# Optimization experiments

Measured on AMD Instinct MI355X. Metric: run time of the kernel, lower is better.

The kernel has to match this reference:

```python
import jax, jax.numpy as jnp
import numpy as np

EMBED_DIM = 128
B, SQ, SKV = 16, 2048, 2048


def setup_inputs() -> dict:
    key = jax.random.key(0)
    ks = jax.random.split(key, 8)
    d = EMBED_DIM
    scale = 1.0 / np.sqrt(d)
    return {
        "x": jax.random.normal(ks[0], (B, SQ, d), dtype=jnp.float32),
        "y": jax.random.normal(ks[1], (B, SKV, d), dtype=jnp.float32),
        "Wq": jax.random.normal(ks[2], (d, d), dtype=jnp.float32) * scale,
        "bq": jax.random.normal(ks[3], (d,), dtype=jnp.float32) * 0.02,
        "Wk": jax.random.normal(ks[4], (d, d), dtype=jnp.float32) * scale,
        "bk": jax.random.normal(ks[5], (d,), dtype=jnp.float32) * 0.02,
        "Wv": jax.random.normal(ks[6], (d, d), dtype=jnp.float32) * scale,
        "bv": jax.random.normal(ks[7], (d,), dtype=jnp.float32) * 0.02,
    }


def reference(x, y, Wq, bq, Wk, bk, Wv, bv):
    # Linear projections (torch Linear: x @ W.T + b; here W stored as [in,out])
    q = x @ Wq + bq            # [B, SQ, d]
    k = y @ Wk + bk            # [B, SKV, d]
    v = y @ Wv + bv            # [B, SKV, d]
    # Source scales by q.size(-1)**0.5 = sqrt(embed_dim)
    inv_scale = 1.0 / jnp.sqrt(jnp.asarray(q.shape[-1], q.dtype))
    scores = jnp.einsum("bqd,bkd->bqk", q, k) * inv_scale  # [B, SQ, SKV]
    attn = jax.nn.softmax(scores, axis=-1)
    return jnp.einsum("bqk,bkd->bqd", attn, v)
```

## Files before the change

### kernel.cpp

```cpp
#include <hip/hip_runtime.h>
#include <hip/hip_bf16.h>

typedef unsigned short ushort_t;
typedef __attribute__((ext_vector_type(8))) short short8;
typedef __attribute__((ext_vector_type(4))) float f32x4;
typedef __attribute__((ext_vector_type(16))) float f32x16;

#define MFMA16(a, b, c) __builtin_amdgcn_mfma_f32_16x16x32_bf16((a), (b), (c), 0, 0, 0)
#define MFMA32(a, b, c) __builtin_amdgcn_mfma_f32_32x32x16_bf16((a), (b), (c), 0, 0, 0)

__device__ __forceinline__ ushort_t f2bf(float f) {
    return __builtin_bit_cast(ushort_t, __float2bfloat16(f));
}

#define CVTPK(lo, hi) ({ unsigned int r_; \
    asm("v_cvt_pk_bf16_f32 %0, %1, %2" : "=v"(r_) : "v"(lo), "v"(hi)); r_; })

__device__ __forceinline__ void gl_lds16(const void* g, void* l) {
    __builtin_amdgcn_global_load_lds((const __attribute__((address_space(1))) void*)g,
                                     (__attribute__((address_space(3))) void*)l, 16, 0, 0);
}

__global__ __launch_bounds__(256) void wt_kernel(
    const float* __restrict__ Wq, const float* __restrict__ Wk, const float* __restrict__ Wv,
    ushort_t* __restrict__ WTq, ushort_t* __restrict__ WTk, ushort_t* __restrict__ WTv)
{
    __shared__ __align__(16) ushort_t wt2[128 * 24];

    const int mat  = blockIdx.x >> 3;
    const int slab = blockIdx.x & 7;
    const float* W = (mat == 0) ? Wq : (mat == 1) ? Wk : Wv;
    ushort_t*   WT = (mat == 0) ? WTq : (mat == 1) ? WTk : WTv;

    const int t = threadIdx.x;
    #pragma unroll
    for (int i = 0; i < 2; ++i) {
        int idx = t + i * 256;
        int kloc = idx >> 5;
        int c0   = (idx & 31) * 4;
        f32x4 v = ((const f32x4*)(W + (size_t)(slab * 16) * 128))[idx];
        #pragma unroll
        for (int j = 0; j < 4; ++j)
            wt2[(c0 + j) * 24 + kloc] = f2bf(v[j]);
    }
    __syncthreads();
    const int r    = t >> 1;
    const int half = t & 1;
    short8 v8 = *(const short8*)&wt2[r * 24 + half * 8];
    *(short8*)(WT + r * 128 + slab * 16 + half * 8) = v8;
}

__global__ __launch_bounds__(256) void proj3(
    const float* __restrict__ x, const float* __restrict__ y,
    const ushort_t* __restrict__ WTq, const float* __restrict__ bq,
    const ushort_t* __restrict__ WTk, const float* __restrict__ bk,
    const ushort_t* __restrict__ WTv, const float* __restrict__ bv,
    ushort_t* __restrict__ Qd, ushort_t* __restrict__ Kd, ushort_t* __restrict__ VTd,
    float qscale)
{
    __shared__ __align__(16) char smem[34816];

    const int t = threadIdx.x;
    const int mat = blockIdx.x >> 9;
    const int pb  = blockIdx.x & 511;
    const float* src = (mat == 0) ? x : y;

    const int w  = t >> 6;
    const int l  = t & 63;
    const int lg = l >> 4;
    const int ln = l & 15;
    const int acol = lg * 8;

    {
        const char* srcb = (const char*)(src + (size_t)(pb * 64) * 128);
        #pragma unroll
        for (int i = 0; i < 8; ++i) {
            int off = i * 4096 + w * 1024 + l * 16;
            int soff = off ^ (((off >> 9) & 7) << 4);
            gl_lds16(srcb + soff, smem + i * 4096 + w * 1024);
        }
    }
    __syncthreads();

    short8 afrag[4];
    {
        const int row = w * 16 + ln;
        const int sw = (row & 7) << 4;
        #pragma unroll
        for (int kc = 0; kc < 4; ++kc) {
            int off0 = row * 512 + lg * 32 + kc * 128;
            f32x4 a0 = *(const f32x4*)(smem + (off0 ^ sw));
            f32x4 a1 = *(const f32x4*)(smem + ((off0 + 16) ^ sw));
            short8 a;
            #pragma unroll
            for (int j = 0; j < 4; ++j) { a[j] = (short)f2bf(a0[j]); a[4 + j] = (short)f2bf(a1[j]); }
            afrag[kc] = a;
        }
    }
    __syncthreads();

    const ushort_t* WT = (mat == 0) ? WTq : (mat == 1) ? WTk : WTv;
    const float*    bb = (mat == 0) ? bq  : (mat == 1) ? bk  : bv;
    const float     sc = (mat == 0) ? qscale : 1.0f;

    if (mat < 2) {
        ushort_t* tile = (ushort_t*)smem;
        #pragma unroll
        for (int ct = 0; ct < 8; ++ct) {
            f32x4 acc = {0.f, 0.f, 0.f, 0.f};
            const int c = ct * 16 + ln;
            #pragma unroll
            for (int kc = 0; kc < 4; ++kc) {
                short8 bfr = *(const short8*)(WT + c * 128 + kc * 32 + acol);
                acc = MFMA16(afrag[kc], bfr, acc);
            }
            float bvv = bb[c];
            #pragma unroll
            for (int reg = 0; reg < 4; ++reg)
                tile[(w * 16 + lg * 4 + reg) * 144 + c] = f2bf((acc[reg] + bvv) * sc);
        }
        __syncthreads();
        const int row = t >> 2, ch = t & 3;
        ushort_t* dst1 = (mat == 0 ? Qd : Kd) + (size_t)(pb * 64 + row) * 128 + ch * 32;
        #pragma unroll
        for (int j = 0; j < 4; ++j)
            *(short8*)(dst1 + j * 8) = *(const short8*)&tile[row * 144 + ch * 32 + j * 8];
    } else {
        ushort_t* vt = (ushort_t*)smem;
        #pragma unroll
        for (int ct = 0; ct < 8; ++ct) {
            f32x4 acc = {0.f, 0.f, 0.f, 0.f};
            const int c = ct * 16 + ln;
            #pragma unroll
            for (int kc = 0; kc < 4; ++kc) {
                short8 bfr = *(const short8*)(WT + c * 128 + kc * 32 + acol);
                acc = MFMA16(afrag[kc], bfr, acc);
            }
            float bvv = bb[c];
            #pragma unroll
            for (int reg = 0; reg < 4; ++reg) {
                int rloc = w * 16 + lg * 4 + reg;
                int byte = (c * 128 + rloc * 2) ^ ((c & 7) << 4);
                *(ushort_t*)((char*)vt + byte) = f2bf(acc[reg] + bvv);
            }
        }
        __syncthreads();
        const int r0b = pb * 64;
        const int b   = r0b >> 11;
        const int kv0 = r0b & 2047;
        const int c    = t >> 1;
        const int half = t & 1;
        ushort_t* dst = VTd + (size_t)b * 128 * 2048 + (size_t)c * 2048 + kv0 + half * 32;
        #pragma unroll
        for (int j = 0; j < 4; ++j) {
            int byte = (c * 128 + (half * 32 + j * 8) * 2) ^ ((c & 7) << 4);
            *(short8*)(dst + j * 8) = *(const short8*)((const char*)vt + byte);
        }
    }
}

#define KVBLK 64
#define NT (2048 / KVBLK)
__global__ __launch_bounds__(256) void attn_kernel(
    const ushort_t* __restrict__ Q, const ushort_t* __restrict__ K,
    const ushort_t* __restrict__ VT, float* __restrict__ out)
{
    __shared__ __align__(16) char smem_[49152];

    const int t = threadIdx.x;
    const int bid = (int)blockIdx.x;
    const int wg = (bid & 7) * 64 + (bid >> 3);
    const int b  = wg >> 5;
    const int q0blk = (wg & 31) * 64;

    const char* Kb  = (const char*)(K  + (size_t)b * 2048 * 128);
    const char* VTb = (const char*)(VT + (size_t)b * 128 * 2048);
    const ushort_t* Qb = Q + (size_t)b * 2048 * 128;

    const int w   = t >> 6;
    const int qg  = w >> 1;
    const int kvh = w & 1;
    const int l  = t & 63;
    const int lq = l & 31;
    const int h  = l >> 5;
    const int q0 = q0blk + qg * 32;

    short8 qfrag[8];
    {
        const ushort_t* qp = Qb + (size_t)(q0 + lq) * 128 + h * 8;
        #pragma unroll
        for (int kc = 0; kc < 8; ++kc)
            qfrag[kc] = *(const short8*)(qp + kc * 16);
    }

    f32x16 o[4];
    #pragma unroll
    for (int db = 0; db < 4; ++db)
        #pragma unroll
        for (int i = 0; i < 16; ++i) o[db][i] = 0.f;
    f32x16 ls;
    #pragma unroll
    for (int i = 0; i < 16; ++i) ls[i] = 0.f;

    auto stageK = [&](char* kd, int kt) {
        const char* kb = Kb + (size_t)kt * KVBLK * 256;
        #pragma unroll
        for (int i = 0; i < 4; ++i) {
            int base = w * 4096 + i * 1024;
            int p = base + l * 16;
            int pl = p ^ (((p >> 8) & 15) << 4);
            gl_lds16(kb + pl, kd + base);
        }
    };
    auto stageV = [&](char* vd, int kt) {
        const int kv2 = kt * KVBLK * 2;
        #pragma unroll
        for (int i = 0; i < 4; ++i) {
            int base = w * 4096 + i * 1024;
            int p = base + l * 16;
            int pl = p ^ (((p >> 8) & 15) << 4);
            int dv = ((pl >> 8) << 1) | ((pl >> 7) & 1);
            gl_lds16(VTb + (size_t)dv * 4096 + kv2 + (pl & 127), vd + base);
        }
    };

    char* bK = smem_;
    char* bV = smem_ + 16384;
    char* bN = smem_ + 32768;

    stageK(bK, 0);
    stageV(bV, 0);

    for (int kt = 0; kt < NT; ++kt) {
        const int ktn = (kt + 1 < NT) ? kt + 1 : 0;

        asm volatile("s_waitcnt vmcnt(4)" ::: "memory");
        __builtin_amdgcn_s_barrier();
        stageK(bN, ktn);

        f32x16 s;
        #pragma unroll
        for (int i = 0; i < 16; ++i) s[i] = 0.f;
        const int krow = kvh * 32 + lq;
        const int ksw = (krow & 15) << 4;
        __builtin_amdgcn_s_setprio(1);
        #pragma unroll
        for (int kc = 0; kc < 8; ++kc) {
            int col = (h * 16 + kc * 32) ^ ksw;
            short8 kf = *(const short8*)(bK + krow * 256 + col);
            s = MFMA32(kf, qfrag[kc], s);
        }
        __builtin_amdgcn_s_setprio(0);

        #pragma unroll
        for (int i = 0; i < 16; ++i) s[i] = __builtin_exp2f(s[i]);
        #pragma unroll
        for (int i = 0; i < 16; ++i) ls[i] += s[i];

        short8 pf[2];
        {
            auto pack2 = [&](int a, short8& outf) {
                unsigned u0 = CVTPK(s[a * 8 + 0], s[a * 8 + 1]);
                unsigned u1 = CVTPK(s[a * 8 + 2], s[a * 8 + 3]);
                unsigned u2 = CVTPK(s[a * 8 + 4], s[a * 8 + 5]);
                unsigned u3 = CVTPK(s[a * 8 + 6], s[a * 8 + 7]);
                asm("v_permlane32_swap_b32 %0, %1" : "+v"(u0), "+v"(u2));
                asm("v_permlane32_swap_b32 %0, %1" : "+v"(u1), "+v"(u3));
                union { unsigned wds[4]; short8 s8; } f;
                f.wds[0] = u0; f.wds[1] = u1; f.wds[2] = u2; f.wds[3] = u3;
                outf = f.s8;
            };
            pack2(0, pf[0]);
            pack2(1, pf[1]);
        }

        asm volatile("s_waitcnt vmcnt(4)" ::: "memory");
        __builtin_amdgcn_s_barrier();
        stageV(bK, ktn);

        __builtin_amdgcn_s_setprio(1);
        #pragma unroll
        for (int db = 0; db < 4; ++db) {
            int d = db * 32 + lq;
            int vrow = d >> 1;
            int vsw = (vrow & 15) << 4;
            #pragma unroll
            for (int ks = 0; ks < 2; ++ks) {
                int colb = ((d & 1) << 7) | (kvh * 64 + ks * 32 + h * 16);
                short8 vf = *(const short8*)(bV + vrow * 256 + (colb ^ vsw));
                o[db] = MFMA32(vf, pf[ks], o[db]);
            }
        }
        __builtin_amdgcn_s_setprio(0);

        char* tmp = bK; bK = bN; bN = bV; bV = tmp;
    }

    asm volatile("s_waitcnt vmcnt(0)" ::: "memory");

    float lsum;
    {
        float a8[8];
        #pragma unroll
        for (int i = 0; i < 8; ++i) a8[i] = ls[i] + ls[i + 8];
        #pragma unroll
        for (int i = 0; i < 4; ++i) a8[i] += a8[i + 4];
        lsum = (a8[0] + a8[1]) + (a8[2] + a8[3]);
    }
    lsum += __shfl_xor(lsum, 32);

    __syncthreads();
    float* mrg = (float*)smem_;
    const int mo = qg * 4224 + lq * 132;
    const int mlb = 8448;

    if (kvh == 1) {
        #pragma unroll
        for (int db = 0; db < 4; ++db) {
            #pragma unroll
            for (int rq = 0; rq < 4; ++rq) {
                f32x4 v4;
                #pragma unroll
                for (int j = 0; j < 4; ++j) v4[j] = o[db][rq * 4 + j];
                *(f32x4*)&mrg[mo + db * 32 + rq * 8 + 4 * h] = v4;
            }
        }
        if (h == 0) mrg[mlb + qg * 64 + lq] = lsum;
    }
    __syncthreads();
    if (kvh == 0) {
        float inv = 1.0f / (lsum + mrg[mlb + qg * 64 + lq]);
        float* ob = out + (size_t)b * 2048 * 128 + (size_t)(q0 + lq) * 128;
        #pragma unroll
        for (int db = 0; db < 4; ++db) {
            #pragma unroll
            for (int rq = 0; rq < 4; ++rq) {
                f32x4 p4 = *(const f32x4*)&mrg[mo + db * 32 + rq * 8 + 4 * h];
                f32x4 st;
                #pragma unroll
                for (int j = 0; j < 4; ++j)
                    st[j] = (o[db][rq * 4 + j] + p4[j]) * inv;
                *(f32x4*)(ob + db * 32 + rq * 8 + 4 * h) = st;
            }
        }
    }
}

extern "C" void kernel_launch(void* const* d_in, const int* in_sizes, int n_in,
                              void* d_out, int out_size, void* d_ws, size_t ws_size,
                              hipStream_t stream) {
    (void)in_sizes; (void)n_in; (void)out_size; (void)ws_size;
    const float* x  = (const float*)d_in[0];
    const float* y  = (const float*)d_in[1];
    const float* Wq = (const float*)d_in[2];
    const float* bq = (const float*)d_in[3];
    const float* Wk = (const float*)d_in[4];
    const float* bk = (const float*)d_in[5];
    const float* Wv = (const float*)d_in[6];
    const float* bv = (const float*)d_in[7];
    float* out = (float*)d_out;

    ushort_t* wtq = (ushort_t*)d_out;
    ushort_t* wtk = wtq + 16384;
    ushort_t* wtv = wtk + 16384;

    ushort_t* qws  = (ushort_t*)d_ws;
    ushort_t* kws  = qws + (size_t)32768 * 128;
    ushort_t* vtws = kws + (size_t)32768 * 128;

    const float qscale = (float)(1.4426950408889634 / 11.313708498984761);

    wt_kernel<<<24, 256, 0, stream>>>(Wq, Wk, Wv, wtq, wtk, wtv);
    proj3<<<1536, 256, 0, stream>>>(x, y, wtq, bq, wtk, bk, wtv, bv, qws, kws, vtws, qscale);
    attn_kernel<<<512, 256, 0, stream>>>(qws, kws, vtws, out);
}
```

Baseline: 95.49 us.

## Fuse weight transpose, projections and attention into one persistent kernel

Merges the three launches (weight transpose, QKV projection, attention) into a single 512-block kernel separated by software grid barriers built on atomic counters, with each block handling three projection jobs in a loop. The goal is to remove launch overhead and the idle gaps between dependent kernels. In exchange it adds a memset launch for the counters and two global barriers that spin with sleeps. It also depends on all 512 blocks being co-resident, which is not guaranteed and could deadlock or time out otherwise. Projection work now runs at 512-block parallelism instead of 1536, and the fallback counter location sits inside the output buffer.

```diff
diff --git a/kernel.cpp b/kernel.cpp
--- a/kernel.cpp
+++ b/kernel.cpp
@@ -21,161 +21,177 @@
                                      (__attribute__((address_space(3))) void*)l, 16, 0, 0);
 }
 
-__global__ __launch_bounds__(256) void wt_kernel(
-    const float* __restrict__ Wq, const float* __restrict__ Wk, const float* __restrict__ Wv,
-    ushort_t* __restrict__ WTq, ushort_t* __restrict__ WTk, ushort_t* __restrict__ WTv)
-{
-    __shared__ __align__(16) ushort_t wt2[128 * 24];
-
-    const int mat  = blockIdx.x >> 3;
-    const int slab = blockIdx.x & 7;
-    const float* W = (mat == 0) ? Wq : (mat == 1) ? Wk : Wv;
-    ushort_t*   WT = (mat == 0) ? WTq : (mat == 1) ? WTk : WTv;
-
-    const int t = threadIdx.x;
-    #pragma unroll
-    for (int i = 0; i < 2; ++i) {
-        int idx = t + i * 256;
-        int kloc = idx >> 5;
-        int c0   = (idx & 31) * 4;
-        f32x4 v = ((const f32x4*)(W + (size_t)(slab * 16) * 128))[idx];
-        #pragma unroll
-        for (int j = 0; j < 4; ++j)
-            wt2[(c0 + j) * 24 + kloc] = f2bf(v[j]);
-    }
+__device__ __forceinline__ void grid_barrier(unsigned* cnt, unsigned target) {
+    __threadfence();
     __syncthreads();
-    const int r    = t >> 1;
-    const int half = t & 1;
-    short8 v8 = *(const short8*)&wt2[r * 24 + half * 8];
-    *(short8*)(WT + r * 128 + slab * 16 + half * 8) = v8;
-}
-
-__global__ __launch_bounds__(256) void proj3(
-    const float* __restrict__ x, const float* __restrict__ y,
-    const ushort_t* __restrict__ WTq, const float* __restrict__ bq,
-    const ushort_t* __restrict__ WTk, const float* __restrict__ bk,
-    const ushort_t* __restrict__ WTv, const float* __restrict__ bv,
-    ushort_t* __restrict__ Qd, ushort_t* __restrict__ Kd, ushort_t* __restrict__ VTd,
-    float qscale)
-{
-    __shared__ __align__(16) char smem[34816];
-
-    const int t = threadIdx.x;
-    const int mat = blockIdx.x >> 9;
-    const int pb  = blockIdx.x & 511;
-    const float* src = (mat == 0) ? x : y;
-
-    const int w  = t >> 6;
-    const int l  = t & 63;
-    const int lg = l >> 4;
-    const int ln = l & 15;
-    const int acol = lg * 8;
-
-    {
-        const char* srcb = (const char*)(src + (size_t)(pb * 64) * 128);
-        #pragma unroll
-        for (int i = 0; i < 8; ++i) {
-            int off = i * 4096 + w * 1024 + l * 16;
-            int soff = off ^ (((off >> 9) & 7) << 4);
-            gl_lds16(srcb + soff, smem + i * 4096 + w * 1024);
+    if (threadIdx.x == 0) {
+        __hip_atomic_fetch_add(cnt, 1u, __ATOMIC_ACQ_REL, __HIP_MEMORY_SCOPE_AGENT);
+        long spins = 0;
+        while (__hip_atomic_load(cnt, __ATOMIC_ACQUIRE, __HIP_MEMORY_SCOPE_AGENT) < target
+               && ++spins < (1L << 28)) {
+            __builtin_amdgcn_s_sleep(8);
         }
     }
     __syncthreads();
-
-    short8 afrag[4];
-    {
-        const int row = w * 16 + ln;
-        const int sw = (row & 7) << 4;
-        #pragma unroll
-        for (int kc = 0; kc < 4; ++kc) {
-            int off0 = row * 512 + lg * 32 + kc * 128;
-            f32x4 a0 = *(const f32x4*)(smem + (off0 ^ sw));
-            f32x4 a1 = *(const f32x4*)(smem + ((off0 + 16) ^ sw));
-            short8 a;
-            #pragma unroll
-            for (int j = 0; j < 4; ++j) { a[j] = (short)f2bf(a0[j]); a[4 + j] = (short)f2bf(a1[j]); }
-            afrag[kc] = a;
-        }
-    }
-    __syncthreads();
-
-    const ushort_t* WT = (mat == 0) ? WTq : (mat == 1) ? WTk : WTv;
-    const float*    bb = (mat == 0) ? bq  : (mat == 1) ? bk  : bv;
-    const float     sc = (mat == 0) ? qscale : 1.0f;
-
-    if (mat < 2) {
-        ushort_t* tile = (ushort_t*)smem;
-        #pragma unroll
-        for (int ct = 0; ct < 8; ++ct) {
-            f32x4 acc = {0.f, 0.f, 0.f, 0.f};
-            const int c = ct * 16 + ln;
-            #pragma unroll
-            for (int kc = 0; kc < 4; ++kc) {
-                short8 bfr = *(const short8*)(WT + c * 128 + kc * 32 + acol);
-                acc = MFMA16(afrag[kc], bfr, acc);
-            }
-            float bvv = bb[c];
-            #pragma unroll
-            for (int reg = 0; reg < 4; ++reg)
-                tile[(w * 16 + lg * 4 + reg) * 144 + c] = f2bf((acc[reg] + bvv) * sc);
-        }
-        __syncthreads();
-        const int row = t >> 2, ch = t & 3;
-        ushort_t* dst1 = (mat == 0 ? Qd : Kd) + (size_t)(pb * 64 + row) * 128 + ch * 32;
-        #pragma unroll
-        for (int j = 0; j < 4; ++j)
-            *(short8*)(dst1 + j * 8) = *(const short8*)&tile[row * 144 + ch * 32 + j * 8];
-    } else {
-        ushort_t* vt = (ushort_t*)smem;
-        #pragma unroll
-        for (int ct = 0; ct < 8; ++ct) {
-            f32x4 acc = {0.f, 0.f, 0.f, 0.f};
-            const int c = ct * 16 + ln;
-            #pragma unroll
-            for (int kc = 0; kc < 4; ++kc) {
-                short8 bfr = *(const short8*)(WT + c * 128 + kc * 32 + acol);
-                acc = MFMA16(afrag[kc], bfr, acc);
-            }
-            float bvv = bb[c];
-            #pragma unroll
-            for (int reg = 0; reg < 4; ++reg) {
-                int rloc = w * 16 + lg * 4 + reg;
-                int byte = (c * 128 + rloc * 2) ^ ((c & 7) << 4);
-                *(ushort_t*)((char*)vt + byte) = f2bf(acc[reg] + bvv);
-            }
-        }
-        __syncthreads();
-        const int r0b = pb * 64;
-        const int b   = r0b >> 11;
-        const int kv0 = r0b & 2047;
-        const int c    = t >> 1;
-        const int half = t & 1;
-        ushort_t* dst = VTd + (size_t)b * 128 * 2048 + (size_t)c * 2048 + kv0 + half * 32;
-        #pragma unroll
-        for (int j = 0; j < 4; ++j) {
-            int byte = (c * 128 + (half * 32 + j * 8) * 2) ^ ((c & 7) << 4);
-            *(short8*)(dst + j * 8) = *(const short8*)((const char*)vt + byte);
-        }
-    }
+    __threadfence();
 }
 
 #define KVBLK 64
 #define NT (2048 / KVBLK)
-__global__ __launch_bounds__(256) void attn_kernel(
-    const ushort_t* __restrict__ Q, const ushort_t* __restrict__ K,
-    const ushort_t* __restrict__ VT, float* __restrict__ out)
+
+__global__ __launch_bounds__(256) void fused_kernel(
+    const float* __restrict__ x, const float* __restrict__ y,
+    const float* __restrict__ Wq, const float* __restrict__ bq,
+    const float* __restrict__ Wk, const float* __restrict__ bk,
+    const float* __restrict__ Wv, const float* __restrict__ bv,
+    ushort_t* __restrict__ WT,
+    ushort_t* __restrict__ Qd, ushort_t* __restrict__ Kd, ushort_t* __restrict__ VTd,
+    float* __restrict__ out, unsigned* __restrict__ cnt, float qscale)
 {
     __shared__ __align__(16) char smem_[49152];
 
     const int t = threadIdx.x;
     const int bid = (int)blockIdx.x;
+
+    if (bid < 24) {
+        ushort_t* wt2 = (ushort_t*)smem_;
+        const int mat  = bid >> 3;
+        const int slab = bid & 7;
+        const float* W = (mat == 0) ? Wq : (mat == 1) ? Wk : Wv;
+        ushort_t*   WTm = WT + mat * 16384;
+
+        #pragma unroll
+        for (int i = 0; i < 2; ++i) {
+            int idx = t + i * 256;
+            int kloc = idx >> 5;
+            int c0   = (idx & 31) * 4;
+            f32x4 v = ((const f32x4*)(W + (size_t)(slab * 16) * 128))[idx];
+            #pragma unroll
+            for (int j = 0; j < 4; ++j)
+                wt2[(c0 + j) * 24 + kloc] = f2bf(v[j]);
+        }
+        __syncthreads();
+        const int r    = t >> 1;
+        const int half = t & 1;
+        short8 v8 = *(const short8*)&wt2[r * 24 + half * 8];
+        *(short8*)(WTm + r * 128 + slab * 16 + half * 8) = v8;
+    }
+
+    grid_barrier(&cnt[0], 512);
+
+    {
+        const int w  = t >> 6;
+        const int l  = t & 63;
+        const int lg = l >> 4;
+        const int ln = l & 15;
+        const int acol = lg * 8;
+
+        for (int j = 0; j < 3; ++j) {
+            const int job = bid + j * 512;
+            const int mat = job >> 9;
+            const int pb  = job & 511;
+            const float* src = (mat == 0) ? x : y;
+
+            __syncthreads();
+
+            {
+                const char* srcb = (const char*)(src + (size_t)(pb * 64) * 128);
+                #pragma unroll
+                for (int i = 0; i < 8; ++i) {
+                    int off = i * 4096 + w * 1024 + l * 16;
+                    int soff = off ^ (((off >> 9) & 7) << 4);
+                    gl_lds16(srcb + soff, smem_ + i * 4096 + w * 1024);
+                }
+            }
+            __syncthreads();
+
+            short8 afrag[4];
+            {
+                const int row = w * 16 + ln;
+                const int sw = (row & 7) << 4;
+                #pragma unroll
+                for (int kc = 0; kc < 4; ++kc) {
+                    int off0 = row * 512 + lg * 32 + kc * 128;
+                    f32x4 a0 = *(const f32x4*)(smem_ + (off0 ^ sw));
+                    f32x4 a1 = *(const f32x4*)(smem_ + ((off0 + 16) ^ sw));
+                    short8 a;
+                    #pragma unroll
+                    for (int jj = 0; jj < 4; ++jj) { a[jj] = (short)f2bf(a0[jj]); a[4 + jj] = (short)f2bf(a1[jj]); }
+                    afrag[kc] = a;
+                }
+            }
+            __syncthreads();
+
+            const ushort_t* WTm = WT + mat * 16384;
+            const float*    bb = (mat == 0) ? bq : (mat == 1) ? bk : bv;
+            const float     sc = (mat == 0) ? qscale : 1.0f;
+
+            if (mat < 2) {
+                ushort_t* tile = (ushort_t*)smem_;
+                #pragma unroll
+                for (int ct = 0; ct < 8; ++ct) {
+                    f32x4 acc = {0.f, 0.f, 0.f, 0.f};
+                    const int c = ct * 16 + ln;
+                    #pragma unroll
+                    for (int kc = 0; kc < 4; ++kc) {
+                        short8 bfr = *(const short8*)(WTm + c * 128 + kc * 32 + acol);
+                        acc = MFMA16(afrag[kc], bfr, acc);
+                    }
+                    float bvv = bb[c];
+                    #pragma unroll
+                    for (int reg = 0; reg < 4; ++reg)
+                        tile[(w * 16 + lg * 4 + reg) * 144 + c] = f2bf((acc[reg] + bvv) * sc);
+                }
+                __syncthreads();
+                const int row = t >> 2, ch = t & 3;
+                ushort_t* dst1 = (mat == 0 ? Qd : Kd) + (size_t)(pb * 64 + row) * 128 + ch * 32;
+                #pragma unroll
+                for (int jj = 0; jj < 4; ++jj)
+                    *(short8*)(dst1 + jj * 8) = *(const short8*)&tile[row * 144 + ch * 32 + jj * 8];
+            } else {
+                ushort_t* vt = (ushort_t*)smem_;
+                #pragma unroll
+                for (int ct = 0; ct < 8; ++ct) {
+                    f32x4 acc = {0.f, 0.f, 0.f, 0.f};
+                    const int c = ct * 16 + ln;
+                    #pragma unroll
+                    for (int kc = 0; kc < 4; ++kc) {
+                        short8 bfr = *(const short8*)(WTm + c * 128 + kc * 32 + acol);
+                        acc = MFMA16(afrag[kc], bfr, acc);
+                    }
+                    float bvv = bb[c];
+                    #pragma unroll
+                    for (int reg = 0; reg < 4; ++reg) {
+                        int rloc = w * 16 + lg * 4 + reg;
+                        int byte = (c * 128 + rloc * 2) ^ ((c & 7) << 4);
+                        *(ushort_t*)((char*)vt + byte) = f2bf(acc[reg] + bvv);
+                    }
+                }
+                __syncthreads();
+                const int r0b = pb * 64;
+                const int b   = r0b >> 11;
+                const int kv0 = r0b & 2047;
+                const int c    = t >> 1;
+                const int half = t & 1;
+                ushort_t* dst = VTd + (size_t)b * 128 * 2048 + (size_t)c * 2048 + kv0 + half * 32;
+                #pragma unroll
+                for (int jj = 0; jj < 4; ++jj) {
+                    int byte = (c * 128 + (half * 32 + jj * 8) * 2) ^ ((c & 7) << 4);
+                    *(short8*)(dst + jj * 8) = *(const short8*)((const char*)vt + byte);
+                }
+            }
+        }
+    }
+
+    grid_barrier(&cnt[1], 512);
+
     const int wg = (bid & 7) * 64 + (bid >> 3);
     const int b  = wg >> 5;
     const int q0blk = (wg & 31) * 64;
 
-    const char* Kb  = (const char*)(K  + (size_t)b * 2048 * 128);
-    const char* VTb = (const char*)(VT + (size_t)b * 128 * 2048);
-    const ushort_t* Qb = Q + (size_t)b * 2048 * 128;
+    const char* Kb  = (const char*)(Kd  + (size_t)b * 2048 * 128);
+    const char* VTb = (const char*)(VTd + (size_t)b * 128 * 2048);
+    const ushort_t* Qb = Qd + (size_t)b * 2048 * 128;
 
     const int w   = t >> 6;
     const int qg  = w >> 1;
@@ -349,7 +365,7 @@
 extern "C" void kernel_launch(void* const* d_in, const int* in_sizes, int n_in,
                               void* d_out, int out_size, void* d_ws, size_t ws_size,
                               hipStream_t stream) {
-    (void)in_sizes; (void)n_in; (void)out_size; (void)ws_size;
+    (void)in_sizes; (void)n_in; (void)out_size;
     const float* x  = (const float*)d_in[0];
     const float* y  = (const float*)d_in[1];
     const float* Wq = (const float*)d_in[2];
@@ -360,17 +376,22 @@
     const float* bv = (const float*)d_in[7];
     float* out = (float*)d_out;
 
-    ushort_t* wtq = (ushort_t*)d_out;
-    ushort_t* wtk = wtq + 16384;
-    ushort_t* wtv = wtk + 16384;
-
     ushort_t* qws  = (ushort_t*)d_ws;
     ushort_t* kws  = qws + (size_t)32768 * 128;
     ushort_t* vtws = kws + (size_t)32768 * 128;
+    const size_t used = (size_t)3 * 32768 * 128 * sizeof(ushort_t);
+    unsigned* cnt;
+    if (ws_size >= used + 256) {
+        cnt = (unsigned*)((char*)d_ws + used);
+    } else {
+        cnt = (unsigned*)((char*)d_out + 196608);
+    }
+
+    ushort_t* wt = (ushort_t*)d_out;
 
     const float qscale = (float)(1.4426950408889634 / 11.313708498984761);
 
-    wt_kernel<<<24, 256, 0, stream>>>(Wq, Wk, Wv, wtq, wtk, wtv);
-    proj3<<<1536, 256, 0, stream>>>(x, y, wtq, bq, wtk, bk, wtv, bv, qws, kws, vtws, qscale);
-    attn_kernel<<<512, 256, 0, stream>>>(qws, kws, vtws, out);
-}
+    hipMemsetAsync(cnt, 0, 8, stream);
+    fused_kernel<<<512, 256, 0, stream>>>(x, y, Wq, bq, Wk, bk, Wv, bv,
+                                          wt, qws, kws, vtws, out, cnt, qscale);
+}
```

Measured after the change: 321.3 us. +236.5%, slower.

## Fuse weight transpose into projection and deepen attention K/V prefetch pipeline

Applied to the files above, without the earlier changes.

Removes the separate weight-transpose kernel. Each projection block now converts and transposes the full fp32 weight matrix into swizzled bf16 LDS itself, which saves one launch but repeats that work in all 1536 blocks and raises LDS to 64KB. The attention kernel goes from a 3-buffer to a 5-buffer rotation, prefetching K/V two tiles ahead with a looser vmcnt wait to hide global-load latency. This raises attention LDS to 80KB, which may cut the number of blocks resident per CU.

```diff
diff --git a/kernel.cpp b/kernel.cpp
--- a/kernel.cpp
+++ b/kernel.cpp
@@ -21,49 +21,23 @@
                                      (__attribute__((address_space(3))) void*)l, 16, 0, 0);
 }
 
-__global__ __launch_bounds__(256) void wt_kernel(
-    const float* __restrict__ Wq, const float* __restrict__ Wk, const float* __restrict__ Wv,
-    ushort_t* __restrict__ WTq, ushort_t* __restrict__ WTk, ushort_t* __restrict__ WTv)
-{
-    __shared__ __align__(16) ushort_t wt2[128 * 24];
-
-    const int mat  = blockIdx.x >> 3;
-    const int slab = blockIdx.x & 7;
-    const float* W = (mat == 0) ? Wq : (mat == 1) ? Wk : Wv;
-    ushort_t*   WT = (mat == 0) ? WTq : (mat == 1) ? WTk : WTv;
-
-    const int t = threadIdx.x;
-    #pragma unroll
-    for (int i = 0; i < 2; ++i) {
-        int idx = t + i * 256;
-        int kloc = idx >> 5;
-        int c0   = (idx & 31) * 4;
-        f32x4 v = ((const f32x4*)(W + (size_t)(slab * 16) * 128))[idx];
-        #pragma unroll
-        for (int j = 0; j < 4; ++j)
-            wt2[(c0 + j) * 24 + kloc] = f2bf(v[j]);
-    }
-    __syncthreads();
-    const int r    = t >> 1;
-    const int half = t & 1;
-    short8 v8 = *(const short8*)&wt2[r * 24 + half * 8];
-    *(short8*)(WT + r * 128 + slab * 16 + half * 8) = v8;
-}
-
 __global__ __launch_bounds__(256) void proj3(
     const float* __restrict__ x, const float* __restrict__ y,
-    const ushort_t* __restrict__ WTq, const float* __restrict__ bq,
-    const ushort_t* __restrict__ WTk, const float* __restrict__ bk,
-    const ushort_t* __restrict__ WTv, const float* __restrict__ bv,
+    const float* __restrict__ Wq, const float* __restrict__ bq,
+    const float* __restrict__ Wk, const float* __restrict__ bk,
+    const float* __restrict__ Wv, const float* __restrict__ bv,
     ushort_t* __restrict__ Qd, ushort_t* __restrict__ Kd, ushort_t* __restrict__ VTd,
     float qscale)
 {
-    __shared__ __align__(16) char smem[34816];
+    __shared__ __align__(16) char smem[65536];
 
     const int t = threadIdx.x;
     const int mat = blockIdx.x >> 9;
     const int pb  = blockIdx.x & 511;
     const float* src = (mat == 0) ? x : y;
+    const float* W   = (mat == 0) ? Wq : (mat == 1) ? Wk : Wv;
+    const float* bb  = (mat == 0) ? bq : (mat == 1) ? bk : bv;
+    const float  sc  = (mat == 0) ? qscale : 1.0f;
 
     const int w  = t >> 6;
     const int l  = t & 63;
@@ -80,6 +54,21 @@
             gl_lds16(srcb + soff, smem + i * 4096 + w * 1024);
         }
     }
+
+    char* wt = smem + 32768;
+    #pragma unroll
+    for (int i = 0; i < 16; ++i) {
+        int idx = t + i * 256;
+        int k  = idx >> 5;
+        int c0 = (idx & 31) * 4;
+        f32x4 v = ((const f32x4*)W)[idx];
+        #pragma unroll
+        for (int j = 0; j < 4; ++j) {
+            int c = c0 + j;
+            int byte = (c * 256 + k * 2) ^ ((c & 7) << 4);
+            *(ushort_t*)(wt + byte) = f2bf(v[j]);
+        }
+    }
     __syncthreads();
 
     short8 afrag[4];
@@ -99,10 +88,6 @@
     }
     __syncthreads();
 
-    const ushort_t* WT = (mat == 0) ? WTq : (mat == 1) ? WTk : WTv;
-    const float*    bb = (mat == 0) ? bq  : (mat == 1) ? bk  : bv;
-    const float     sc = (mat == 0) ? qscale : 1.0f;
-
     if (mat < 2) {
         ushort_t* tile = (ushort_t*)smem;
         #pragma unroll
@@ -111,7 +96,8 @@
             const int c = ct * 16 + ln;
             #pragma unroll
             for (int kc = 0; kc < 4; ++kc) {
-                short8 bfr = *(const short8*)(WT + c * 128 + kc * 32 + acol);
+                int byte = (c * 256 + (kc * 32 + acol) * 2) ^ ((c & 7) << 4);
+                short8 bfr = *(const short8*)(wt + byte);
                 acc = MFMA16(afrag[kc], bfr, acc);
             }
             float bvv = bb[c];
@@ -133,7 +119,8 @@
             const int c = ct * 16 + ln;
             #pragma unroll
             for (int kc = 0; kc < 4; ++kc) {
-                short8 bfr = *(const short8*)(WT + c * 128 + kc * 32 + acol);
+                int byte = (c * 256 + (kc * 32 + acol) * 2) ^ ((c & 7) << 4);
+                short8 bfr = *(const short8*)(wt + byte);
                 acc = MFMA16(afrag[kc], bfr, acc);
             }
             float bvv = bb[c];
@@ -165,7 +152,7 @@
     const ushort_t* __restrict__ Q, const ushort_t* __restrict__ K,
     const ushort_t* __restrict__ VT, float* __restrict__ out)
 {
-    __shared__ __align__(16) char smem_[49152];
+    __shared__ __align__(16) char smem_[81920];
 
     const int t = threadIdx.x;
     const int bid = (int)blockIdx.x;
@@ -224,19 +211,23 @@
         }
     };
 
-    char* bK = smem_;
-    char* bV = smem_ + 16384;
-    char* bN = smem_ + 32768;
-
-    stageK(bK, 0);
-    stageV(bV, 0);
+    char* p0 = smem_;
+    char* p1 = smem_ + 16384;
+    char* p2 = smem_ + 32768;
+    char* p3 = smem_ + 49152;
+    char* p4 = smem_ + 65536;
+
+    stageK(p0, 0);
+    stageV(p1, 0);
+    stageK(p2, 1);
+    stageV(p3, 1);
 
     for (int kt = 0; kt < NT; ++kt) {
-        const int ktn = (kt + 1 < NT) ? kt + 1 : 0;
-
-        asm volatile("s_waitcnt vmcnt(4)" ::: "memory");
+        const int kt2 = (kt + 2 < NT) ? kt + 2 : 0;
+
+        asm volatile("s_waitcnt vmcnt(12)" ::: "memory");
         __builtin_amdgcn_s_barrier();
-        stageK(bN, ktn);
+        stageK(p4, kt2);
 
         f32x16 s;
         #pragma unroll
@@ -247,7 +238,7 @@
         #pragma unroll
         for (int kc = 0; kc < 8; ++kc) {
             int col = (h * 16 + kc * 32) ^ ksw;
-            short8 kf = *(const short8*)(bK + krow * 256 + col);
+            short8 kf = *(const short8*)(p0 + krow * 256 + col);
             s = MFMA32(kf, qfrag[kc], s);
         }
         __builtin_amdgcn_s_setprio(0);
@@ -274,9 +265,9 @@
             pack2(1, pf[1]);
         }
 
-        asm volatile("s_waitcnt vmcnt(4)" ::: "memory");
+        asm volatile("s_waitcnt vmcnt(12)" ::: "memory");
         __builtin_amdgcn_s_barrier();
-        stageV(bK, ktn);
+        stageV(p0, kt2);
 
         __builtin_amdgcn_s_setprio(1);
         #pragma unroll
@@ -287,13 +278,14 @@
             #pragma unroll
             for (int ks = 0; ks < 2; ++ks) {
                 int colb = ((d & 1) << 7) | (kvh * 64 + ks * 32 + h * 16);
-                short8 vf = *(const short8*)(bV + vrow * 256 + (colb ^ vsw));
+                short8 vf = *(const short8*)(p1 + vrow * 256 + (colb ^ vsw));
                 o[db] = MFMA32(vf, pf[ks], o[db]);
             }
         }
         __builtin_amdgcn_s_setprio(0);
 
-        char* tmp = bK; bK = bN; bN = bV; bV = tmp;
+        char* n0 = p2; char* n1 = p3; char* n2 = p4; char* n3 = p0; char* n4 = p1;
+        p0 = n0; p1 = n1; p2 = n2; p3 = n3; p4 = n4;
     }
 
     asm volatile("s_waitcnt vmcnt(0)" ::: "memory");
@@ -335,11 +327,11 @@
         for (int db = 0; db < 4; ++db) {
             #pragma unroll
             for (int rq = 0; rq < 4; ++rq) {
-                f32x4 p4 = *(const f32x4*)&mrg[mo + db * 32 + rq * 8 + 4 * h];
+                f32x4 p4v = *(const f32x4*)&mrg[mo + db * 32 + rq * 8 + 4 * h];
                 f32x4 st;
                 #pragma unroll
                 for (int j = 0; j < 4; ++j)
-                    st[j] = (o[db][rq * 4 + j] + p4[j]) * inv;
+                    st[j] = (o[db][rq * 4 + j] + p4v[j]) * inv;
                 *(f32x4*)(ob + db * 32 + rq * 8 + 4 * h) = st;
             }
         }
@@ -360,17 +352,12 @@
     const float* bv = (const float*)d_in[7];
     float* out = (float*)d_out;
 
-    ushort_t* wtq = (ushort_t*)d_out;
-    ushort_t* wtk = wtq + 16384;
-    ushort_t* wtv = wtk + 16384;
-
     ushort_t* qws  = (ushort_t*)d_ws;
     ushort_t* kws  = qws + (size_t)32768 * 128;
     ushort_t* vtws = kws + (size_t)32768 * 128;
 
     const float qscale = (float)(1.4426950408889634 / 11.313708498984761);
 
-    wt_kernel<<<24, 256, 0, stream>>>(Wq, Wk, Wv, wtq, wtk, wtv);
-    proj3<<<1536, 256, 0, stream>>>(x, y, wtq, bq, wtk, bk, wtv, bv, qws, kws, vtws, qscale);
+    proj3<<<1536, 256, 0, stream>>>(x, y, Wq, bq, Wk, bk, Wv, bv, qws, kws, vtws, qscale);
     attn_kernel<<<512, 256, 0, stream>>>(qws, kws, vtws, out);
 }
```

Result: no change. 94.21 us (-1.3%).
